# Performance work log

Measured on AMD Instinct MI355X. Metric: run time of the kernel, lower is better.

Reference implementation:

```python
import jax, jax.numpy as jnp
import numpy as np

B, P, L, H, HA = 32, 128, 19, 256, 128
SLOPE = 0.2
NEG = -1e9


def setup_inputs() -> dict:
    key = jax.random.key(0)
    k1, k2, k3, k4, k5 = jax.random.split(key, 5)
    agents = jax.random.normal(k1, (B, P, L, H), dtype=jnp.float32)
    adj = jax.random.normal(k2, (B, P, P, L), dtype=jnp.float32)
    mask = jax.random.randint(k3, (B, P), 0, 2) == 1
    # xavier_uniform-style scale (gain=1.414)
    W1 = jax.random.normal(k4, (HA, H), dtype=jnp.float32) * (1.414 / np.sqrt(H))
    W2 = jax.random.normal(k5, (1, 2 * HA), dtype=jnp.float32) * (1.414 / np.sqrt(2 * HA))
    return {"agents": agents, "adj": adj, "mask": mask, "W1": W1, "W2": W2}


def reference(agents, adj, mask, W1, W2):
    # agents: (B,P,L,H), adj: (B,P,P,L), mask: (B,P) bool
    Wag = jnp.einsum('bplh,ah->bpla', agents, W1)          # linear1, (B,P,L,HA)
    # linear2 on cat([att1, att2]) decomposes: score_ij = Wag_i @ w2a + Wag_j @ w2b
    w2a = W2[0, :HA]
    w2b = W2[0, HA:]
    e_i = Wag @ w2a                                         # (B,P,L)
    e_j = Wag @ w2b                                         # (B,P,L)
    logits = jax.nn.leaky_relu(e_i[:, :, None, :] + e_j[:, None, :, :], SLOPE)  # (B,P,P,L)
    logits = jnp.where(mask[:, None, :, None], NEG, logits)
    att = jax.nn.softmax(logits, axis=2)                    # softmax over neighbor j
    # mode 'HSA': adj gate = (adj > 0) * 1.0 ; dropout p=0 -> identity
    weights = att * (adj > 0.0).astype(agents.dtype)        # (B,P,P,L)
    out = jax.nn.sigmoid(jnp.einsum('bijl,bjlh->bilh', weights, agents))
    return out
```

## Files before the change

kernel.cpp:

```cpp
#include <hip/hip_runtime.h>
#include <math.h>

#define B  32
#define P  128
#define L  19
#define H  256
#define SLOPE 0.2f
#define PL (P*L)
#define LH (L*H)
#define PLH (P*L*H)
#define NBLK (B*L)

#define WW  136
#define ABW 136

typedef __attribute__((ext_vector_type(8))) short bf16x8;
typedef __attribute__((ext_vector_type(4))) float f32x4;

__device__ inline unsigned short f32_to_bf16(float x) {
    unsigned u = __builtin_bit_cast(unsigned, x);
    unsigned r = (u + 0x7fffu + ((u >> 16) & 1u)) >> 16;
    return (unsigned short)r;
}
__device__ inline unsigned pack_bf16x2(float f0, float f1) {
    return (unsigned)f32_to_bf16(f0) | ((unsigned)f32_to_bf16(f1) << 16);
}

__global__ __launch_bounds__(256) void prep(
    const float* __restrict__ adj,
    const unsigned char* __restrict__ m,
    const float* __restrict__ W1,
    const float* __restrict__ W2,
    unsigned* __restrict__ bits,
    int* __restrict__ flag,
    float* __restrict__ u)
{
    int blk = blockIdx.x;
    if (blk < B*P) {
        __shared__ unsigned char f[PL];
        int b = blk >> 7, i = blk & 127;
        const float4* row = (const float4*)(adj + (size_t)blk * PL);
        for (int q = threadIdx.x; q < PL/4; q += 256) {
            float4 v = row[q];
            f[q*4]   = v.x > 0.f;
            f[q*4+1] = v.y > 0.f;
            f[q*4+2] = v.z > 0.f;
            f[q*4+3] = v.w > 0.f;
        }
        __syncthreads();
        int t = threadIdx.x;
        if (t < 76) {
            int l = t >> 2, jw = t & 3;
            unsigned wv = 0;
            #pragma unroll
            for (int k = 0; k < 32; ++k)
                wv |= (unsigned)f[(jw*32 + k)*L + l] << k;
            bits[(((size_t)b*L + l)*P + i)*4 + jw] = wv;
        }
    } else {
        __shared__ int s;
        if (threadIdx.x == 0) s = 0;
        __syncthreads();
        int acc = 0;
        for (int k = threadIdx.x; k < 1024; k += 256)
            acc |= m[4*k+1] | m[4*k+2] | m[4*k+3];
        if (acc) atomicOr(&s, 1);
        __syncthreads();
        if (threadIdx.x == 0) flag[0] = s;
        int h = threadIdx.x;
        float s1 = 0.f, s2 = 0.f;
        for (int a = 0; a < 128; ++a) {
            float wv = W1[a*H + h];
            s1 += wv * W2[a];
            s2 += wv * W2[128 + a];
        }
        u[h]     = s1;
        u[H + h] = s2;
    }
}

__global__ __launch_bounds__(512, 6) void gat_main(
    const float* __restrict__ A,
    const unsigned* __restrict__ bits,
    const void*  __restrict__ maskp,
    const int*   __restrict__ flagp,
    const float* __restrict__ u,
    float* __restrict__ out)
{
    __shared__ unsigned short W[P*WW];
    __shared__ unsigned short Ab[32*ABW];
    __shared__ unsigned bitw[P*4];
    __shared__ __align__(16) float u_lds[2*H];
    __shared__ float e2f[P];
    __shared__ float e2c[P];
    __shared__ float e1s[P];
    __shared__ float invs[P];
    __shared__ int   joff[P];
    __shared__ int   cnt[2];

    int w   = blockIdx.x;
    int xcd = w & 7;
    int q   = w >> 3;
    int l   = q % 19;
    int bg  = q / 19;
    int b   = bg*8 + xcd;
    int tid = threadIdx.x;

    int flag = flagp[0];
    int keep = 0;
    if (tid < P) {
        int mv = flag ? (((const unsigned char*)maskp)[b*P + tid] != 0)
                      : (((const int*)maskp)[b*P + tid] != 0);
        keep = !mv;
    }
    unsigned long long bal = __ballot(keep);
    if (tid == 0)  cnt[0] = (int)__popcll(bal);
    if (tid == 64) cnt[1] = (int)__popcll(bal);
    bitw[tid]  = bits[(((size_t)b*L + l)*P)*4 + tid];
    u_lds[tid] = u[tid];
    __syncthreads();
    int M  = cnt[0] + cnt[1];
    int Kn = (M + 31) >> 5;
    if (keep) {
        int lane = tid & 63;
        int pos  = (int)__popcll(bal & ((1ull << lane) - 1ull));
        if (tid >= 64) pos += cnt[0];
        joff[pos] = tid;
    }

    {
        int j = tid >> 2, c = tid & 3;
        const float* ar = A + (size_t)b*PLH + (size_t)j*LH + (size_t)l*H;
        float s1 = 0.f, s2 = 0.f;
        #pragma unroll
        for (int t = 0; t < 16; ++t) {
            int o = (t*4 + c)*4;
            float4 a  = *(const float4*)(ar + o);
            float4 v1 = *(const float4*)&u_lds[o];
            float4 v2 = *(const float4*)&u_lds[H + o];
            s1 += a.x*v1.x + a.y*v1.y + a.z*v1.z + a.w*v1.w;
            s2 += a.x*v2.x + a.y*v2.y + a.z*v2.z + a.w*v2.w;
        }
        s1 += __shfl_xor(s1, 1, 4); s1 += __shfl_xor(s1, 2, 4);
        s2 += __shfl_xor(s2, 1, 4); s2 += __shfl_xor(s2, 2, 4);
        if (c == 0) { e1s[j] = s1; e2f[j] = s2; }
    }
    __syncthreads();

    if (tid < P) {
        int jsrc = (tid < M) ? joff[tid] : joff[M-1];
        if (tid >= M) joff[tid] = jsrc;
        e2c[tid] = e2f[jsrc];
    }
    __syncthreads();

    auto stage = [&](int qh) {
        int h_s = tid & 31;
        int jq  = tid >> 5;
        int sw  = ((h_s >> 3) & 3) << 1;
        const float* abase = A + (size_t)b*PLH + (size_t)l*H + qh*32 + h_s;
        for (int o = jq; o < Kn*4; o += 16) {
            unsigned pk[4];
            #pragma unroll
            for (int t = 0; t < 4; ++t) {
                float f0 = abase[(size_t)joff[o*8 + 2*t]     * LH];
                float f1 = abase[(size_t)joff[o*8 + 2*t + 1] * LH];
                pk[t] = pack_bf16x2(f0, f1);
            }
            *(uint4*)&Ab[h_s*ABW + (o ^ sw)*8] = make_uint4(pk[0], pk[1], pk[2], pk[3]);
        }
    };

    stage(0);

    {
        int i  = tid >> 2;
        int jl = tid & 3;
        float e1v = e1s[i];
        float mx = -INFINITY;
        for (int jj = jl; jj < M; jj += 4) mx = fmaxf(mx, e2c[jj]);
        mx = fmaxf(mx, __shfl_xor(mx, 1, 4));
        mx = fmaxf(mx, __shfl_xor(mx, 2, 4));
        float s0 = e1v + mx;
        float m  = fmaxf(s0, SLOPE*s0);
        float sum = 0.f;
        for (int jj = jl; jj < Kn*32; jj += 4) {
            if (jj < M) {
                int j   = joff[jj];
                float s = e1v + e2c[jj];
                s = fmaxf(s, SLOPE*s);
                float ex = __expf(s - m);
                sum += ex;
                unsigned bit = (bitw[i*4 + (j >> 5)] >> (j & 31)) & 1u;
                W[i*WW + jj] = bit ? f32_to_bf16(ex) : (unsigned short)0;
            } else {
                W[i*WW + jj] = 0;
            }
        }
        sum += __shfl_xor(sum, 1, 4);
        sum += __shfl_xor(sum, 2, 4);
        if (jl == 0) invs[i] = 1.f / sum;
    }
    __syncthreads();

    int lane = tid & 63;
    int wv   = tid >> 6;
    int fr   = lane & 15;
    int kc   = lane >> 4;

    bf16x8 af[4];
    #pragma unroll
    for (int ks = 0; ks < 4; ++ks)
        if (ks < Kn) af[ks] = *(const bf16x8*)&W[(wv*16 + fr)*WW + ks*32 + kc*8];

    float inv4[4];
    #pragma unroll
    for (int rr = 0; rr < 4; ++rr) inv4[rr] = invs[wv*16 + kc*4 + rr];

    for (int qh = 0; qh < 8; ++qh) {
        #pragma unroll
        for (int ht = 0; ht < 2; ++ht) {
            int row = ht*16 + fr;
            int sw  = ((row >> 3) & 3) << 1;
            f32x4 acc = {0.f, 0.f, 0.f, 0.f};
            #pragma unroll
            for (int ks = 0; ks < 4; ++ks) {
                if (ks < Kn) {
                    bf16x8 bf = *(const bf16x8*)&Ab[row*ABW + ((ks*4 + kc) ^ sw)*8];
                    acc = __builtin_amdgcn_mfma_f32_16x16x32_bf16(af[ks], bf, acc, 0, 0, 0);
                }
            }
            int hcol = qh*32 + ht*16 + fr;
            float* op = out + ((size_t)(b*P + wv*16 + kc*4)*L + l)*H + hcol;
            #pragma unroll
            for (int rr = 0; rr < 4; ++rr) {
                float x = acc[rr] * inv4[rr];
                op[(size_t)rr*LH] = 1.f/(1.f + __expf(-x));
            }
        }
        if (qh < 7) {
            __syncthreads();
            stage(qh + 1);
            __syncthreads();
        }
    }
}

extern "C" void kernel_launch(void* const* d_in, const int* in_sizes, int n_in,
                              void* d_out, int out_size, void* d_ws, size_t ws_size,
                              hipStream_t stream) {
    const float* agents = (const float*)d_in[0];
    const float* adj    = (const float*)d_in[1];
    const void*  mask   = d_in[2];
    const float* W1     = (const float*)d_in[3];
    const float* W2     = (const float*)d_in[4];
    float* out = (float*)d_out;

    int*      flag = (int*)d_ws;
    float*    u    = (float*)d_ws + 16;
    unsigned* bits = (unsigned*)(u + 2*H);

    prep    <<<B*P + 1, 256, 0, stream>>>(adj, (const unsigned char*)mask,
                                          W1, W2, bits, flag, u);
    gat_main<<<NBLK, 512, 0, stream>>>(agents, bits, mask, flag, u, out);
}
```

Baseline: 56.21 us.

## Split rows across two blocks and double-buffer agent staging through registers

Each (b,l) block is split into two 256-thread blocks that each own 64 query rows, which doubles the grid and improves occupancy. Staging of the next 32-column agent slice is now double-buffered: global loads go into registers before the MFMA work and are written to the alternate LDS buffer afterwards, so each step needs one barrier instead of two. The sigmoid now uses a hardware reciprocal. The cost is that each half-block recomputes the e1/e2 projections and re-gathers the same agent columns, which doubles that gather traffic.

```diff
diff --git a/kernel.cpp b/kernel.cpp
--- a/kernel.cpp
+++ b/kernel.cpp
@@ -9,7 +9,7 @@
 #define PL (P*L)
 #define LH (L*H)
 #define PLH (P*L*H)
-#define NBLK (B*L)
+#define NBLK (B*L*2)
 
 #define WW  136
 #define ABW 136
@@ -79,7 +79,7 @@
     }
 }
 
-__global__ __launch_bounds__(512, 6) void gat_main(
+__global__ __launch_bounds__(256, 4) void gat_main(
     const float* __restrict__ A,
     const unsigned* __restrict__ bits,
     const void*  __restrict__ maskp,
@@ -87,24 +87,27 @@
     const float* __restrict__ u,
     float* __restrict__ out)
 {
-    __shared__ unsigned short W[P*WW];
-    __shared__ unsigned short Ab[32*ABW];
-    __shared__ unsigned bitw[P*4];
+    __shared__ unsigned short W[64*WW];
+    __shared__ unsigned short Ab[2][32*ABW];
+    __shared__ unsigned bitw[64*4];
     __shared__ __align__(16) float u_lds[2*H];
+    __shared__ float e1f[P];
     __shared__ float e2f[P];
     __shared__ float e2c[P];
-    __shared__ float e1s[P];
-    __shared__ float invs[P];
+    __shared__ float invs[64];
     __shared__ int   joff[P];
     __shared__ int   cnt[2];
 
-    int w   = blockIdx.x;
-    int xcd = w & 7;
-    int q   = w >> 3;
-    int l   = q % 19;
-    int bg  = q / 19;
-    int b   = bg*8 + xcd;
-    int tid = threadIdx.x;
+    int w     = blockIdx.x;
+    int xcd   = w & 7;
+    int idx   = w >> 3;
+    int ihalf = idx & 1;
+    int q     = idx >> 1;
+    int l     = q % 19;
+    int bg    = q / 19;
+    int b     = bg*8 + xcd;
+    int i0h   = ihalf*64;
+    int tid   = threadIdx.x;
 
     int flag = flagp[0];
     int keep = 0;
@@ -116,11 +119,13 @@
     unsigned long long bal = __ballot(keep);
     if (tid == 0)  cnt[0] = (int)__popcll(bal);
     if (tid == 64) cnt[1] = (int)__popcll(bal);
-    bitw[tid]  = bits[(((size_t)b*L + l)*P)*4 + tid];
-    u_lds[tid] = u[tid];
-    __syncthreads();
-    int M  = cnt[0] + cnt[1];
-    int Kn = (M + 31) >> 5;
+    bitw[tid]       = bits[(((size_t)b*L + l)*P + i0h)*4 + tid];
+    u_lds[tid]      = u[tid];
+    u_lds[tid+256]  = u[tid+256];
+    __syncthreads();
+    int M   = cnt[0] + cnt[1];
+    int Kn  = (M + 31) >> 5;
+    int Kn4 = Kn * 4;
     if (keep) {
         int lane = tid & 63;
         int pos  = (int)__popcll(bal & ((1ull << lane) - 1ull));
@@ -129,21 +134,21 @@
     }
 
     {
-        int j = tid >> 2, c = tid & 3;
+        int j = tid >> 1, c = tid & 1;
         const float* ar = A + (size_t)b*PLH + (size_t)j*LH + (size_t)l*H;
         float s1 = 0.f, s2 = 0.f;
         #pragma unroll
-        for (int t = 0; t < 16; ++t) {
-            int o = (t*4 + c)*4;
+        for (int t = 0; t < 32; ++t) {
+            int o = (t*2 + c)*4;
             float4 a  = *(const float4*)(ar + o);
             float4 v1 = *(const float4*)&u_lds[o];
             float4 v2 = *(const float4*)&u_lds[H + o];
             s1 += a.x*v1.x + a.y*v1.y + a.z*v1.z + a.w*v1.w;
             s2 += a.x*v2.x + a.y*v2.y + a.z*v2.z + a.w*v2.w;
         }
-        s1 += __shfl_xor(s1, 1, 4); s1 += __shfl_xor(s1, 2, 4);
-        s2 += __shfl_xor(s2, 1, 4); s2 += __shfl_xor(s2, 2, 4);
-        if (c == 0) { e1s[j] = s1; e2f[j] = s2; }
+        s1 += __shfl_xor(s1, 1, 2);
+        s2 += __shfl_xor(s2, 1, 2);
+        if (c == 0) { e1f[j] = s1; e2f[j] = s2; }
     }
     __syncthreads();
 
@@ -154,29 +159,43 @@
     }
     __syncthreads();
 
-    auto stage = [&](int qh) {
-        int h_s = tid & 31;
-        int jq  = tid >> 5;
-        int sw  = ((h_s >> 3) & 3) << 1;
-        const float* abase = A + (size_t)b*PLH + (size_t)l*H + qh*32 + h_s;
-        for (int o = jq; o < Kn*4; o += 16) {
-            unsigned pk[4];
-            #pragma unroll
-            for (int t = 0; t < 4; ++t) {
-                float f0 = abase[(size_t)joff[o*8 + 2*t]     * LH];
-                float f1 = abase[(size_t)joff[o*8 + 2*t + 1] * LH];
-                pk[t] = pack_bf16x2(f0, f1);
-            }
-            *(uint4*)&Ab[h_s*ABW + (o ^ sw)*8] = make_uint4(pk[0], pk[1], pk[2], pk[3]);
+    int h_s = tid & 31;
+    int jq  = tid >> 5;
+    int sw  = ((h_s >> 3) & 3) << 1;
+    const float* abase = A + (size_t)b*PLH + (size_t)l*H + h_s;
+    float rg[2][8];
+
+    auto stage_load = [&](int qh) {
+        #pragma unroll
+        for (int cc = 0; cc < 2; ++cc) {
+            int o = jq + cc*8;
+            if (o < Kn4) {
+                #pragma unroll
+                for (int t = 0; t < 8; ++t)
+                    rg[cc][t] = abase[(size_t)joff[o*8 + t]*LH + qh*32];
+            }
         }
     };
-
-    stage(0);
+    auto stage_write = [&](int buf) {
+        #pragma unroll
+        for (int cc = 0; cc < 2; ++cc) {
+            int o = jq + cc*8;
+            if (o < Kn4) {
+                unsigned p0 = pack_bf16x2(rg[cc][0], rg[cc][1]);
+                unsigned p1 = pack_bf16x2(rg[cc][2], rg[cc][3]);
+                unsigned p2 = pack_bf16x2(rg[cc][4], rg[cc][5]);
+                unsigned p3 = pack_bf16x2(rg[cc][6], rg[cc][7]);
+                *(uint4*)&Ab[buf][h_s*ABW + (o ^ sw)*8] = make_uint4(p0, p1, p2, p3);
+            }
+        }
+    };
+
+    stage_load(0);
 
     {
-        int i  = tid >> 2;
+        int il = tid >> 2;
         int jl = tid & 3;
-        float e1v = e1s[i];
+        float e1v = e1f[i0h + il];
         float mx = -INFINITY;
         for (int jj = jl; jj < M; jj += 4) mx = fmaxf(mx, e2c[jj]);
         mx = fmaxf(mx, __shfl_xor(mx, 1, 4));
@@ -191,16 +210,18 @@
                 s = fmaxf(s, SLOPE*s);
                 float ex = __expf(s - m);
                 sum += ex;
-                unsigned bit = (bitw[i*4 + (j >> 5)] >> (j & 31)) & 1u;
-                W[i*WW + jj] = bit ? f32_to_bf16(ex) : (unsigned short)0;
+                unsigned bit = (bitw[il*4 + (j >> 5)] >> (j & 31)) & 1u;
+                W[il*WW + jj] = bit ? f32_to_bf16(ex) : (unsigned short)0;
             } else {
-                W[i*WW + jj] = 0;
+                W[il*WW + jj] = 0;
             }
         }
         sum += __shfl_xor(sum, 1, 4);
         sum += __shfl_xor(sum, 2, 4);
-        if (jl == 0) invs[i] = 1.f / sum;
-    }
+        if (jl == 0) invs[il] = 1.f / sum;
+    }
+    __syncthreads();
+    stage_write(0);
     __syncthreads();
 
     int lane = tid & 63;
@@ -218,31 +239,31 @@
     for (int rr = 0; rr < 4; ++rr) inv4[rr] = invs[wv*16 + kc*4 + rr];
 
     for (int qh = 0; qh < 8; ++qh) {
+        if (qh < 7) stage_load(qh + 1);
+        int buf = qh & 1;
         #pragma unroll
         for (int ht = 0; ht < 2; ++ht) {
             int row = ht*16 + fr;
-            int sw  = ((row >> 3) & 3) << 1;
+            int swr = ((row >> 3) & 3) << 1;
             f32x4 acc = {0.f, 0.f, 0.f, 0.f};
             #pragma unroll
             for (int ks = 0; ks < 4; ++ks) {
                 if (ks < Kn) {
-                    bf16x8 bf = *(const bf16x8*)&Ab[row*ABW + ((ks*4 + kc) ^ sw)*8];
+                    bf16x8 bf = *(const bf16x8*)&Ab[buf][row*ABW + ((ks*4 + kc) ^ swr)*8];
                     acc = __builtin_amdgcn_mfma_f32_16x16x32_bf16(af[ks], bf, acc, 0, 0, 0);
                 }
             }
             int hcol = qh*32 + ht*16 + fr;
-            float* op = out + ((size_t)(b*P + wv*16 + kc*4)*L + l)*H + hcol;
+            float* op = out + ((size_t)(b*P + i0h + wv*16 + kc*4)*L + l)*H + hcol;
             #pragma unroll
             for (int rr = 0; rr < 4; ++rr) {
                 float x = acc[rr] * inv4[rr];
-                op[(size_t)rr*LH] = 1.f/(1.f + __expf(-x));
-            }
-        }
-        if (qh < 7) {
-            __syncthreads();
-            stage(qh + 1);
-            __syncthreads();
-        }
+                float e = __expf(-x);
+                op[(size_t)rr*LH] = __builtin_amdgcn_rcpf(1.f + e);
+            }
+        }
+        if (qh < 7) stage_write(buf ^ 1);
+        __syncthreads();
     }
 }
 
@@ -262,5 +283,5 @@
 
     prep    <<<B*P + 1, 256, 0, stream>>>(adj, (const unsigned char*)mask,
                                           W1, W2, bits, flag, u);
-    gat_main<<<NBLK, 512, 0, stream>>>(agents, bits, mask, flag, u, out);
-}
+    gat_main<<<NBLK, 256, 0, stream>>>(agents, bits, mask, flag, u, out);
+}
```

Result: slower. 63.45 us (+12.9%).

## Double-buffer agent staging with register prefetch, reusing weight LDS as second buffer

Applied to the files above, without the earlier changes.

The per-chunk staging of agent columns into LDS now uses two buffers, with the second one aliased onto the attention-weight array once its fragments are held in registers. The global loads for the next chunk are issued into registers before the current chunk's MFMAs and written to LDS afterwards. This cuts one barrier per step and lets gather latency overlap with compute and the output stores. The sigmoid's division is also replaced with a hardware reciprocal. In exchange, register pressure rises and the aliasing depends on every thread having loaded its weight fragments before the first write to that array.

```diff
diff --git a/kernel.cpp b/kernel.cpp
--- a/kernel.cpp
+++ b/kernel.cpp
@@ -87,8 +87,8 @@
     const float* __restrict__ u,
     float* __restrict__ out)
 {
-    __shared__ unsigned short W[P*WW];
-    __shared__ unsigned short Ab[32*ABW];
+    __shared__ __align__(16) unsigned short W[P*WW];
+    __shared__ __align__(16) unsigned short Ab0[32*ABW];
     __shared__ unsigned bitw[P*4];
     __shared__ __align__(16) float u_lds[2*H];
     __shared__ float e2f[P];
@@ -98,6 +98,8 @@
     __shared__ int   joff[P];
     __shared__ int   cnt[2];
 
+    unsigned short* Ab1 = (unsigned short*)W;
+
     int w   = blockIdx.x;
     int xcd = w & 7;
     int q   = w >> 3;
@@ -119,8 +121,9 @@
     bitw[tid]  = bits[(((size_t)b*L + l)*P)*4 + tid];
     u_lds[tid] = u[tid];
     __syncthreads();
-    int M  = cnt[0] + cnt[1];
-    int Kn = (M + 31) >> 5;
+    int M   = cnt[0] + cnt[1];
+    int Kn  = (M + 31) >> 5;
+    int Kn4 = Kn * 4;
     if (keep) {
         int lane = tid & 63;
         int pos  = (int)__popcll(bal & ((1ull << lane) - 1ull));
@@ -154,24 +157,35 @@
     }
     __syncthreads();
 
-    auto stage = [&](int qh) {
-        int h_s = tid & 31;
-        int jq  = tid >> 5;
-        int sw  = ((h_s >> 3) & 3) << 1;
-        const float* abase = A + (size_t)b*PLH + (size_t)l*H + qh*32 + h_s;
-        for (int o = jq; o < Kn*4; o += 16) {
-            unsigned pk[4];
-            #pragma unroll
-            for (int t = 0; t < 4; ++t) {
-                float f0 = abase[(size_t)joff[o*8 + 2*t]     * LH];
-                float f1 = abase[(size_t)joff[o*8 + 2*t + 1] * LH];
-                pk[t] = pack_bf16x2(f0, f1);
-            }
-            *(uint4*)&Ab[h_s*ABW + (o ^ sw)*8] = make_uint4(pk[0], pk[1], pk[2], pk[3]);
+    int h_s = tid & 31;
+    int jq  = tid >> 5;
+    int sw  = ((h_s >> 3) & 3) << 1;
+    const float* abase = A + (size_t)b*PLH + (size_t)l*H + h_s;
+    int   jreg[8];
+    float rg[8];
+    if (jq < Kn4) {
+        #pragma unroll
+        for (int t = 0; t < 8; ++t) jreg[t] = joff[jq*8 + t];
+    }
+
+    auto stage_load = [&](int qh) {
+        if (jq < Kn4) {
+            #pragma unroll
+            for (int t = 0; t < 8; ++t)
+                rg[t] = abase[(size_t)jreg[t]*LH + qh*32];
         }
     };
-
-    stage(0);
+    auto stage_write = [&](unsigned short* ab) {
+        if (jq < Kn4) {
+            unsigned p0 = pack_bf16x2(rg[0], rg[1]);
+            unsigned p1 = pack_bf16x2(rg[2], rg[3]);
+            unsigned p2 = pack_bf16x2(rg[4], rg[5]);
+            unsigned p3 = pack_bf16x2(rg[6], rg[7]);
+            *(uint4*)&ab[h_s*ABW + (jq ^ sw)*8] = make_uint4(p0, p1, p2, p3);
+        }
+    };
+
+    stage_load(0);
 
     {
         int i  = tid >> 2;
@@ -217,16 +231,20 @@
     #pragma unroll
     for (int rr = 0; rr < 4; ++rr) inv4[rr] = invs[wv*16 + kc*4 + rr];
 
-    for (int qh = 0; qh < 8; ++qh) {
+    stage_write(Ab0);
+    __syncthreads();
+
+    auto mfma_step = [&](int qh, const unsigned short* cur, unsigned short* nxt) {
+        if (qh < 7) stage_load(qh + 1);
         #pragma unroll
         for (int ht = 0; ht < 2; ++ht) {
             int row = ht*16 + fr;
-            int sw  = ((row >> 3) & 3) << 1;
+            int swr = ((row >> 3) & 3) << 1;
             f32x4 acc = {0.f, 0.f, 0.f, 0.f};
             #pragma unroll
             for (int ks = 0; ks < 4; ++ks) {
                 if (ks < Kn) {
-                    bf16x8 bf = *(const bf16x8*)&Ab[row*ABW + ((ks*4 + kc) ^ sw)*8];
+                    bf16x8 bf = *(const bf16x8*)&cur[row*ABW + ((ks*4 + kc) ^ swr)*8];
                     acc = __builtin_amdgcn_mfma_f32_16x16x32_bf16(af[ks], bf, acc, 0, 0, 0);
                 }
             }
@@ -235,14 +253,20 @@
             #pragma unroll
             for (int rr = 0; rr < 4; ++rr) {
                 float x = acc[rr] * inv4[rr];
-                op[(size_t)rr*LH] = 1.f/(1.f + __expf(-x));
+                float e = __expf(-x);
+                op[(size_t)rr*LH] = __builtin_amdgcn_rcpf(1.f + e);
             }
         }
         if (qh < 7) {
+            stage_write(nxt);
             __syncthreads();
-            stage(qh + 1);
-            __syncthreads();
-        }
+        }
+    };
+
+    #pragma unroll
+    for (int qp = 0; qp < 4; ++qp) {
+        mfma_step(2*qp,     Ab0, Ab1);
+        mfma_step(2*qp + 1, Ab1, Ab0);
     }
 }
 
```

Measured after the change: 49.60 us, median of 2. 1.13x faster.

## Stage full agents tile once in LDS during score pass, build softmax weights in registers

Applied to the files above, without the earlier changes.

The agents slice for a (batch, l) block is now converted to bf16 and written into a full 256-row LDS tile during the initial e1/e2 dot-product pass, replacing the eight re-staging rounds that gathered from global memory with syncthreads between them. Softmax weights are computed into registers and redistributed to the MFMA A-fragment layout with wave shuffles instead of a W buffer in LDS. The output loop becomes a single pass over 16 column tiles, and the sigmoid uses a fast reciprocal. The larger LDS footprint lowers the occupancy hint from 6 to 4 blocks, and the transposed scalar 16-bit LDS stores may cause bank conflicts.

```diff
diff --git a/kernel.cpp b/kernel.cpp
--- a/kernel.cpp
+++ b/kernel.cpp
@@ -11,19 +11,16 @@
 #define PLH (P*L*H)
 #define NBLK (B*L)
 
-#define WW  136
-#define ABW 136
+#define ABW2 136
 
 typedef __attribute__((ext_vector_type(8))) short bf16x8;
 typedef __attribute__((ext_vector_type(4))) float f32x4;
+typedef __attribute__((ext_vector_type(4))) unsigned uint32x4;
 
 __device__ inline unsigned short f32_to_bf16(float x) {
     unsigned u = __builtin_bit_cast(unsigned, x);
     unsigned r = (u + 0x7fffu + ((u >> 16) & 1u)) >> 16;
     return (unsigned short)r;
-}
-__device__ inline unsigned pack_bf16x2(float f0, float f1) {
-    return (unsigned)f32_to_bf16(f0) | ((unsigned)f32_to_bf16(f1) << 16);
 }
 
 __global__ __launch_bounds__(256) void prep(
@@ -79,7 +76,7 @@
     }
 }
 
-__global__ __launch_bounds__(512, 6) void gat_main(
+__global__ __launch_bounds__(512, 4) void gat_main(
     const float* __restrict__ A,
     const unsigned* __restrict__ bits,
     const void*  __restrict__ maskp,
@@ -87,15 +84,12 @@
     const float* __restrict__ u,
     float* __restrict__ out)
 {
-    __shared__ unsigned short W[P*WW];
-    __shared__ unsigned short Ab[32*ABW];
+    __shared__ __align__(16) unsigned short Ab[256*ABW2];
+    __shared__ __align__(16) float u_lds[2*H];
     __shared__ unsigned bitw[P*4];
-    __shared__ __align__(16) float u_lds[2*H];
-    __shared__ float e2f[P];
+    __shared__ float e1f[P];
     __shared__ float e2c[P];
-    __shared__ float e1s[P];
-    __shared__ float invs[P];
-    __shared__ int   joff[P];
+    __shared__ int   row_map[P];
     __shared__ int   cnt[2];
 
     int w   = blockIdx.x;
@@ -116,20 +110,30 @@
     unsigned long long bal = __ballot(keep);
     if (tid == 0)  cnt[0] = (int)__popcll(bal);
     if (tid == 64) cnt[1] = (int)__popcll(bal);
+    u_lds[tid] = u[tid];
     bitw[tid]  = bits[(((size_t)b*L + l)*P)*4 + tid];
-    u_lds[tid] = u[tid];
     __syncthreads();
     int M  = cnt[0] + cnt[1];
     int Kn = (M + 31) >> 5;
-    if (keep) {
+    int KT = Kn * 32;
+    if (tid < P) {
         int lane = tid & 63;
-        int pos  = (int)__popcll(bal & ((1ull << lane) - 1ull));
-        if (tid >= 64) pos += cnt[0];
-        joff[pos] = tid;
-    }
+        unsigned long long below = (1ull << lane) - 1ull;
+        if (keep) {
+            int pos = (int)__popcll(bal & below) + (tid >= 64 ? cnt[0] : 0);
+            row_map[pos] = tid;
+        } else {
+            int pos = (int)__popcll(~bal & below) + (tid >= 64 ? 64 - cnt[0] : 0);
+            row_map[M + pos] = tid;
+        }
+    }
+    __syncthreads();
 
     {
-        int j = tid >> 2, c = tid & 3;
+        int g = tid >> 2, c = tid & 3;
+        int j = row_map[g];
+        int stage = (g < M);
+        int gz    = (g < KT);
         const float* ar = A + (size_t)b*PLH + (size_t)j*LH + (size_t)l*H;
         float s1 = 0.f, s2 = 0.f;
         #pragma unroll
@@ -140,108 +144,109 @@
             float4 v2 = *(const float4*)&u_lds[H + o];
             s1 += a.x*v1.x + a.y*v1.y + a.z*v1.z + a.w*v1.w;
             s2 += a.x*v2.x + a.y*v2.y + a.z*v2.z + a.w*v2.w;
+            if (gz) {
+                Ab[(o+0)*ABW2 + g] = stage ? f32_to_bf16(a.x) : (unsigned short)0;
+                Ab[(o+1)*ABW2 + g] = stage ? f32_to_bf16(a.y) : (unsigned short)0;
+                Ab[(o+2)*ABW2 + g] = stage ? f32_to_bf16(a.z) : (unsigned short)0;
+                Ab[(o+3)*ABW2 + g] = stage ? f32_to_bf16(a.w) : (unsigned short)0;
+            }
         }
         s1 += __shfl_xor(s1, 1, 4); s1 += __shfl_xor(s1, 2, 4);
         s2 += __shfl_xor(s2, 1, 4); s2 += __shfl_xor(s2, 2, 4);
-        if (c == 0) { e1s[j] = s1; e2f[j] = s2; }
+        if (c == 0) {
+            e1f[j] = s1;
+            if (stage) e2c[g] = s2;
+        }
     }
     __syncthreads();
 
-    if (tid < P) {
-        int jsrc = (tid < M) ? joff[tid] : joff[M-1];
-        if (tid >= M) joff[tid] = jsrc;
-        e2c[tid] = e2f[jsrc];
-    }
-    __syncthreads();
-
-    auto stage = [&](int qh) {
-        int h_s = tid & 31;
-        int jq  = tid >> 5;
-        int sw  = ((h_s >> 3) & 3) << 1;
-        const float* abase = A + (size_t)b*PLH + (size_t)l*H + qh*32 + h_s;
-        for (int o = jq; o < Kn*4; o += 16) {
-            unsigned pk[4];
-            #pragma unroll
-            for (int t = 0; t < 4; ++t) {
-                float f0 = abase[(size_t)joff[o*8 + 2*t]     * LH];
-                float f1 = abase[(size_t)joff[o*8 + 2*t + 1] * LH];
-                pk[t] = pack_bf16x2(f0, f1);
-            }
-            *(uint4*)&Ab[h_s*ABW + (o ^ sw)*8] = make_uint4(pk[0], pk[1], pk[2], pk[3]);
-        }
-    };
-
-    stage(0);
-
+    int lane = tid & 63;
+    int wv   = tid >> 6;
+    int fr   = lane & 15;
+    int kc   = lane >> 4;
+
+    unsigned words[4][4];
+    float myinv;
     {
-        int i  = tid >> 2;
-        int jl = tid & 3;
-        float e1v = e1s[i];
+        int i = tid >> 2, c = tid & 3;
+        float e1v = e1f[i];
         float mx = -INFINITY;
-        for (int jj = jl; jj < M; jj += 4) mx = fmaxf(mx, e2c[jj]);
+        for (int jj = c; jj < M; jj += 4) mx = fmaxf(mx, e2c[jj]);
         mx = fmaxf(mx, __shfl_xor(mx, 1, 4));
         mx = fmaxf(mx, __shfl_xor(mx, 2, 4));
         float s0 = e1v + mx;
         float m  = fmaxf(s0, SLOPE*s0);
         float sum = 0.f;
-        for (int jj = jl; jj < Kn*32; jj += 4) {
-            if (jj < M) {
-                int j   = joff[jj];
-                float s = e1v + e2c[jj];
-                s = fmaxf(s, SLOPE*s);
-                float ex = __expf(s - m);
-                sum += ex;
-                unsigned bit = (bitw[i*4 + (j >> 5)] >> (j & 31)) & 1u;
-                W[i*WW + jj] = bit ? f32_to_bf16(ex) : (unsigned short)0;
+        unsigned bw0 = bitw[i*4], bw1 = bitw[i*4+1],
+                 bw2 = bitw[i*4+2], bw3 = bitw[i*4+3];
+        #pragma unroll
+        for (int ks = 0; ks < 4; ++ks) {
+            unsigned short v[8];
+            if (ks < Kn) {
+                #pragma unroll
+                for (int t = 0; t < 8; ++t) {
+                    int jj = ks*32 + c*8 + t;
+                    unsigned short wb = 0;
+                    if (jj < M) {
+                        int j   = row_map[jj];
+                        float s = e1v + e2c[jj];
+                        s = fmaxf(s, SLOPE*s);
+                        float ex = __expf(s - m);
+                        sum += ex;
+                        unsigned sel = (j & 64) ? ((j & 32) ? bw3 : bw2)
+                                                : ((j & 32) ? bw1 : bw0);
+                        unsigned bit = (sel >> (j & 31)) & 1u;
+                        wb = bit ? f32_to_bf16(ex) : (unsigned short)0;
+                    }
+                    v[t] = wb;
+                }
             } else {
-                W[i*WW + jj] = 0;
+                #pragma unroll
+                for (int t = 0; t < 8; ++t) v[t] = 0;
             }
+            words[ks][0] = (unsigned)v[0] | ((unsigned)v[1] << 16);
+            words[ks][1] = (unsigned)v[2] | ((unsigned)v[3] << 16);
+            words[ks][2] = (unsigned)v[4] | ((unsigned)v[5] << 16);
+            words[ks][3] = (unsigned)v[6] | ((unsigned)v[7] << 16);
         }
         sum += __shfl_xor(sum, 1, 4);
         sum += __shfl_xor(sum, 2, 4);
-        if (jl == 0) invs[i] = 1.f / sum;
-    }
-    __syncthreads();
-
-    int lane = tid & 63;
-    int wv   = tid >> 6;
-    int fr   = lane & 15;
-    int kc   = lane >> 4;
+        myinv = 1.f / sum;
+    }
 
     bf16x8 af[4];
+    int sl = ((lane & 15) << 2) | (lane >> 4);
     #pragma unroll
-    for (int ks = 0; ks < 4; ++ks)
-        if (ks < Kn) af[ks] = *(const bf16x8*)&W[(wv*16 + fr)*WW + ks*32 + kc*8];
-
+    for (int ks = 0; ks < 4; ++ks) {
+        uint32x4 uu;
+        uu.x = (unsigned)__shfl((int)words[ks][0], sl, 64);
+        uu.y = (unsigned)__shfl((int)words[ks][1], sl, 64);
+        uu.z = (unsigned)__shfl((int)words[ks][2], sl, 64);
+        uu.w = (unsigned)__shfl((int)words[ks][3], sl, 64);
+        af[ks] = __builtin_bit_cast(bf16x8, uu);
+    }
     float inv4[4];
     #pragma unroll
-    for (int rr = 0; rr < 4; ++rr) inv4[rr] = invs[wv*16 + kc*4 + rr];
-
-    for (int qh = 0; qh < 8; ++qh) {
-        #pragma unroll
-        for (int ht = 0; ht < 2; ++ht) {
-            int row = ht*16 + fr;
-            int sw  = ((row >> 3) & 3) << 1;
-            f32x4 acc = {0.f, 0.f, 0.f, 0.f};
-            #pragma unroll
-            for (int ks = 0; ks < 4; ++ks) {
-                if (ks < Kn) {
-                    bf16x8 bf = *(const bf16x8*)&Ab[row*ABW + ((ks*4 + kc) ^ sw)*8];
-                    acc = __builtin_amdgcn_mfma_f32_16x16x32_bf16(af[ks], bf, acc, 0, 0, 0);
-                }
+    for (int rr = 0; rr < 4; ++rr)
+        inv4[rr] = __shfl(myinv, ((lane >> 4) << 4) | (rr << 2), 64);
+
+    #pragma unroll 4
+    for (int hq = 0; hq < 16; ++hq) {
+        int hrow = hq*16 + fr;
+        f32x4 acc = {0.f, 0.f, 0.f, 0.f};
+        #pragma unroll
+        for (int ks = 0; ks < 4; ++ks) {
+            if (ks < Kn) {
+                bf16x8 bf = *(const bf16x8*)&Ab[hrow*ABW2 + (ks*4 + kc)*8];
+                acc = __builtin_amdgcn_mfma_f32_16x16x32_bf16(af[ks], bf, acc, 0, 0, 0);
             }
-            int hcol = qh*32 + ht*16 + fr;
-            float* op = out + ((size_t)(b*P + wv*16 + kc*4)*L + l)*H + hcol;
-            #pragma unroll
-            for (int rr = 0; rr < 4; ++rr) {
-                float x = acc[rr] * inv4[rr];
-                op[(size_t)rr*LH] = 1.f/(1.f + __expf(-x));
-            }
-        }
-        if (qh < 7) {
-            __syncthreads();
-            stage(qh + 1);
-            __syncthreads();
+        }
+        #pragma unroll
+        for (int rr = 0; rr < 4; ++rr) {
+            float x = acc[rr] * inv4[rr];
+            float e = __expf(-x);
+            out[((size_t)(b*P + wv*16 + kc*4 + rr)*L + l)*H + hrow] =
+                __builtin_amdgcn_rcpf(1.f + e);
         }
     }
 }
```

After: 108.1 us. +92.3%, slower.
